# Kernel optimization log

Measured on AMD Instinct MI355X. Metric: run time of the kernel, lower is better.

## Reference

```python
import jax, jax.numpy as jnp
import numpy as np

N = 100000
D = 128      # embedding_dim
HID = 32     # hidden per head
HEADS = 4
OUT_C = 64
E = 1600000
NEG_SLOPE = 0.2


def setup_inputs() -> dict:
    key = jax.random.key(0)
    ks = jax.random.split(key, 12)
    inp = {}
    inp["x_indices"] = jnp.arange(N, dtype=jnp.int64)
    inp["ei"] = jax.random.randint(ks[0], (2, E), 0, N, dtype=jnp.int64)
    # parameters
    inp["emb"] = jax.random.normal(ks[1], (N, D), dtype=jnp.float32)
    # conv1: in=D, out=HID per head, HEADS heads, concat
    s1 = 1.0 / np.sqrt(D)
    inp["W1"] = jax.random.normal(ks[2], (D, HEADS * HID), dtype=jnp.float32) * s1
    inp["a_src1"] = jax.random.normal(ks[3], (HEADS, HID), dtype=jnp.float32) * s1
    inp["a_dst1"] = jax.random.normal(ks[4], (HEADS, HID), dtype=jnp.float32) * s1
    inp["b1"] = jnp.zeros((HEADS * HID,), dtype=jnp.float32)
    # conv2: in=HEADS*HID, out=OUT_C, 1 head
    s2 = 1.0 / np.sqrt(HEADS * HID)
    inp["W2"] = jax.random.normal(ks[5], (HEADS * HID, OUT_C), dtype=jnp.float32) * s2
    inp["a_src2"] = jax.random.normal(ks[6], (1, OUT_C), dtype=jnp.float32) * s2
    inp["a_dst2"] = jax.random.normal(ks[7], (1, OUT_C), dtype=jnp.float32) * s2
    inp["b2"] = jnp.zeros((OUT_C,), dtype=jnp.float32)
    return inp


def gat_conv(x, src, dst, W, a_src, a_dst, b, heads, out_ch, concat):
    # x: [N, Din]; src/dst: [E'] (self-loops already included)
    n = x.shape[0]
    h = (x @ W).reshape(n, heads, out_ch)          # [N, H, C]
    alpha_s = jnp.sum(h * a_src, axis=-1)          # [N, H]
    alpha_d = jnp.sum(h * a_dst, axis=-1)          # [N, H]
    e = alpha_s[src] + alpha_d[dst]                # [E', H]
    e = jnp.where(e > 0, e, NEG_SLOPE * e)         # leaky_relu
    # segment softmax over incoming edges per destination node
    m = jax.ops.segment_max(e, dst, num_segments=n)      # [N, H]
    ex = jnp.exp(e - m[dst])
    den = jax.ops.segment_sum(ex, dst, num_segments=n)   # [N, H]
    a = ex / den[dst]                              # [E', H]  (self-loops guarantee den>0)
    msg = h[src] * a[:, :, None]                   # [E', H, C]
    out = jax.ops.segment_sum(msg, dst, num_segments=n)  # [N, H, C]
    if concat:
        out = out.reshape(n, heads * out_ch)
    else:
        out = out.mean(axis=1)
    return out + b


def reference(x_indices, ei, emb, W1, a_src1, a_dst1, b1, W2, a_src2, a_dst2, b2):
    n = emb.shape[0]
    # PyG GATConv default add_self_loops=True
    loop = jnp.arange(n, dtype=ei.dtype)
    src = jnp.concatenate([ei[0], loop])
    dst = jnp.concatenate([ei[1], loop])
    x = emb[x_indices]                                  # embedding lookup
    x = jax.nn.elu(gat_conv(x, src, dst, W1, a_src1, a_dst1, b1, HEADS, HID, True))
    # dropout p=0.5 is identity in eval mode
    return gat_conv(x, src, dst, W2, a_src2, a_dst2, b2, 1, OUT_C, True)
```

## Files before the change

kernel.cpp:

```cpp
#include <hip/hip_runtime.h>
#include <math.h>

#define NEG_SLOPE 0.2f
#define BK_SHIFT 8

typedef __attribute__((ext_vector_type(2))) float v2f;

__device__ __forceinline__ float leaky(float x) { return x > 0.f ? x : NEG_SLOPE * x; }
__device__ __forceinline__ float dot4(float4 a, float4 b) {
    return a.x * b.x + a.y * b.y + a.z * b.z + a.w * b.w;
}
__device__ __forceinline__ unsigned short f2bf(float f) {
    unsigned int x = __float_as_uint(f);
    unsigned int r = (x + 0x7fffu + ((x >> 16) & 1u)) >> 16;
    return (unsigned short)r;
}
__device__ __forceinline__ float bflo(unsigned int u) { return __uint_as_float(u << 16); }
__device__ __forceinline__ float bfhi(unsigned int u) { return __uint_as_float(u & 0xffff0000u); }


__global__ void __launch_bounds__(256) bcount_kernel(const int* __restrict__ ei, int E, int E2,
                                                     int K, int* __restrict__ bcounts) {
    __shared__ int h[512];
    int t = threadIdx.x;
    h[t] = 0; h[t + 256] = 0;
    __syncthreads();
    int base = blockIdx.x * 4096;
#pragma unroll 4
    for (int i = 0; i < 16; i++) {
        int e = base + i * 256 + t;
        if (e < E2) {
            int dst = (e < E) ? ei[E + e] : (e - E);
            atomicAdd(&h[dst >> BK_SHIFT], 1);
        }
    }
    __syncthreads();
    for (int b = t; b < K; b += 256) {
        int c = h[b];
        if (c) atomicAdd(&bcounts[b], c);
    }
}

__global__ void __launch_bounds__(512) bscan_kernel(const int* __restrict__ bcounts, int K,
                                                    int* __restrict__ bbase, int* __restrict__ bcursor) {
    __shared__ int s[512];
    int t = threadIdx.x;
    int v = (t < K) ? bcounts[t] : 0;
    s[t] = v;
    __syncthreads();
    for (int off = 1; off < 512; off <<= 1) {
        int u = (t >= off) ? s[t - off] : 0;
        __syncthreads();
        s[t] += u;
        __syncthreads();
    }
    if (t < K) {
        int ex = s[t] - v;
        bbase[t] = ex;
        bcursor[t] = ex;
    }
    if (t == 511) bbase[K] = s[511];
}

__global__ void __launch_bounds__(256) bscatter_kernel(const int* __restrict__ ei, int E, int E2,
                                                       int K, int* __restrict__ bcursor,
                                                       unsigned int* __restrict__ bedges) {
    __shared__ int hist[512], pre[512], lcur[512], gbase[512], psum[256];
    __shared__ unsigned int stage[4096];
    __shared__ unsigned short binof[4096];
    int t = threadIdx.x;
    hist[t] = 0; hist[t + 256] = 0;
    __syncthreads();
    int base = blockIdx.x * 4096;
    int cnt = min(4096, E2 - base);
    int s_[16], d_[16];
#pragma unroll
    for (int i = 0; i < 16; i++) {
        int e = base + i * 256 + t;
        if (e < E2) {
            int ss, dd;
            if (e < E) { ss = ei[e]; dd = ei[E + e]; }
            else       { ss = e - E; dd = ss; }
            s_[i] = ss; d_[i] = dd;
            atomicAdd(&hist[dd >> BK_SHIFT], 1);
        }
    }
    __syncthreads();
    int a0 = hist[2 * t], a1 = hist[2 * t + 1];
    psum[t] = a0 + a1;
    __syncthreads();
    for (int off = 1; off < 256; off <<= 1) {
        int u = (t >= off) ? psum[t - off] : 0;
        __syncthreads();
        psum[t] += u;
        __syncthreads();
    }
    int pex = psum[t] - (a0 + a1);
    pre[2 * t] = pex;
    pre[2 * t + 1] = pex + a0;
    __syncthreads();
    for (int b = t; b < K; b += 256) {
        int c = hist[b];
        if (c) gbase[b] = atomicAdd(&bcursor[b], c);
    }
    lcur[t] = pre[t]; lcur[t + 256] = pre[t + 256];
    __syncthreads();
#pragma unroll
    for (int i = 0; i < 16; i++) {
        int e = base + i * 256 + t;
        if (e < E2) {
            int bin = d_[i] >> BK_SHIFT;
            int p = atomicAdd(&lcur[bin], 1);
            stage[p] = ((unsigned)s_[i] << 8) | (unsigned)(d_[i] & 255);
            binof[p] = (unsigned short)bin;
        }
    }
    __syncthreads();
    for (int i = t; i < cnt; i += 256) {
        unsigned int ed = stage[i];
        int bin = (int)binof[i];
        bedges[gbase[bin] + (i - pre[bin])] = ed;
    }
}

__global__ void __launch_bounds__(256) bcsr_kernel(const unsigned int* __restrict__ bedges,
                                                   const int* __restrict__ bbase, int N,
                                                   int* __restrict__ counts, int* __restrict__ indptr,
                                                   int* __restrict__ csr) {
    __shared__ int hist[256], scn[256], cur[256];
    int b = blockIdx.x;
    int t = threadIdx.x;
    int base = bbase[b];
    int cnt = bbase[b + 1] - base;
    hist[t] = 0;
    __syncthreads();
    for (int i = t; i < cnt; i += 256) {
        atomicAdd(&hist[bedges[base + i] & 255u], 1);
    }
    __syncthreads();
    int v = hist[t];
    scn[t] = v;
    __syncthreads();
    for (int off = 1; off < 256; off <<= 1) {
        int u = (t >= off) ? scn[t - off] : 0;
        __syncthreads();
        scn[t] += u;
        __syncthreads();
    }
    int ex = scn[t] - v;
    int d = (b << BK_SHIFT) + t;
    if (d < N) { counts[d] = v; indptr[d] = base + ex; }
    cur[t] = ex;
    __syncthreads();
    for (int i = t; i < cnt; i += 256) {
        unsigned int ed = bedges[base + i];
        int p = atomicAdd(&cur[ed & 255u], 1);
        csr[base + p] = (int)(ed >> 8);
    }
}


__global__ void w2pack_kernel(const float* __restrict__ W2, unsigned* __restrict__ w2p) {
    int i = blockIdx.x * 256 + threadIdx.x;
    if (i < 4096) {
        int k = i >> 5, j = i & 31;
        w2p[i] = (unsigned)f2bf(W2[k * 64 + 2 * j]) |
                 ((unsigned)f2bf(W2[k * 64 + 2 * j + 1]) << 16);
    }
}


__device__ __forceinline__ void fma16(float4 xv, float4 wv0, float4 wv1,
                                      float4 wv2, float4 wv3, float4& a) {
    a.x = fmaf(xv.x, wv0.x, a.x); a.y = fmaf(xv.x, wv0.y, a.y);
    a.z = fmaf(xv.x, wv0.z, a.z); a.w = fmaf(xv.x, wv0.w, a.w);
    a.x = fmaf(xv.y, wv1.x, a.x); a.y = fmaf(xv.y, wv1.y, a.y);
    a.z = fmaf(xv.y, wv1.z, a.z); a.w = fmaf(xv.y, wv1.w, a.w);
    a.x = fmaf(xv.z, wv2.x, a.x); a.y = fmaf(xv.z, wv2.y, a.y);
    a.z = fmaf(xv.z, wv2.z, a.z); a.w = fmaf(xv.z, wv2.w, a.w);
    a.x = fmaf(xv.w, wv3.x, a.x); a.y = fmaf(xv.w, wv3.y, a.y);
    a.z = fmaf(xv.w, wv3.z, a.z); a.w = fmaf(xv.w, wv3.w, a.w);
}


__global__ __launch_bounds__(256) void gemm1_kernel(const float* __restrict__ emb,
                             const int* __restrict__ xidx,
                             const float* __restrict__ W1,
                             unsigned short* __restrict__ h1b,
                             const float* __restrict__ a_s1, const float* __restrict__ a_d1,
                             float* __restrict__ as1, float* __restrict__ ad1, int N) {
    __shared__ float xs[64][64];
    __shared__ float ws[64][128];
    int tid = threadIdx.x;
    int r0 = blockIdx.x * 64;
    int tr = tid >> 5;
    int tc = tid & 31;
    float4 acc[8];
#pragma unroll
    for (int i = 0; i < 8; i++) acc[i] = make_float4(0.f, 0.f, 0.f, 0.f);
    const float4* W4 = (const float4*)W1;
    const float4* emb4 = (const float4*)emb;
    float4* ws4 = (float4*)ws;
    float4* xs4 = (float4*)xs;

    for (int half = 0; half < 2; half++) {
        float4 wbuf[8];
#pragma unroll
        for (int j = 0; j < 8; j++) wbuf[j] = W4[half * 2048 + tid + j * 256];
        float4 xbuf[4];
#pragma unroll
        for (int j = 0; j < 4; j++) {
            int idx = tid + j * 256;
            int r = idx >> 4, c = idx & 15;
            int row = r0 + r;
            float4 v = make_float4(0.f, 0.f, 0.f, 0.f);
            if (row < N) {
                int s = xidx[row];
                v = emb4[(size_t)s * 32 + half * 16 + c];
            }
            xbuf[j] = v;
        }
        __syncthreads();
#pragma unroll
        for (int j = 0; j < 8; j++) ws4[tid + j * 256] = wbuf[j];
#pragma unroll
        for (int j = 0; j < 4; j++) xs4[tid + j * 256] = xbuf[j];
        __syncthreads();
        for (int k = 0; k < 64; k += 4) {
            float4 wv0 = *(const float4*)&ws[k][tc * 4];
            float4 wv1 = *(const float4*)&ws[k + 1][tc * 4];
            float4 wv2 = *(const float4*)&ws[k + 2][tc * 4];
            float4 wv3 = *(const float4*)&ws[k + 3][tc * 4];
#pragma unroll
            for (int i = 0; i < 8; i++) {
                float4 xv = *(const float4*)&xs[tr * 8 + i][k];
                fma16(xv, wv0, wv1, wv2, wv3, acc[i]);
            }
        }
    }
    int colbase = tc * 4;
    int h = tc >> 3;
    int off = (tc & 7) * 4;
    float4 av = *(const float4*)&a_s1[h * 32 + off];
    float4 dv = *(const float4*)&a_d1[h * 32 + off];
#pragma unroll
    for (int i = 0; i < 8; i++) {
        int row = r0 + tr * 8 + i;
        if (row < N) {
            ushort4 pk;
            pk.x = f2bf(acc[i].x); pk.y = f2bf(acc[i].y);
            pk.z = f2bf(acc[i].z); pk.w = f2bf(acc[i].w);
            *(ushort4*)&h1b[(size_t)row * 128 + colbase] = pk;
        }
        float ps = dot4(acc[i], av);
        float pd = dot4(acc[i], dv);
        ps += __shfl_xor(ps, 1); pd += __shfl_xor(pd, 1);
        ps += __shfl_xor(ps, 2); pd += __shfl_xor(pd, 2);
        ps += __shfl_xor(ps, 4); pd += __shfl_xor(pd, 4);
        if ((tc & 7) == 0 && row < N) {
            as1[row * 4 + h] = ps;
            ad1[row * 4 + h] = pd;
        }
    }
}


__device__ __forceinline__ void edge_fma(uint4 u0, float w, v2f* acc) {
    v2f wv = {w, w};
    v2f t;
    t.x = bflo(u0.x); t.y = bfhi(u0.x); acc[0] += wv * t;
    t.x = bflo(u0.y); t.y = bfhi(u0.y); acc[1] += wv * t;
    t.x = bflo(u0.z); t.y = bfhi(u0.z); acc[2] += wv * t;
    t.x = bflo(u0.w); t.y = bfhi(u0.w); acc[3] += wv * t;
}

__device__ __forceinline__ void accum_tbl1(int srcReg, const float* __restrict__ ew, int mcount,
                                           const uint4* __restrict__ h1v4,
                                           int lanebase, int sub, int cg, int hh, v2f* acc) {
    int b = 0;
    for (; b + 8 <= mcount; b += 8) {
        int i0 = b + sub, i1 = b + 2 + sub, i2 = b + 4 + sub, i3 = b + 6 + sub;
        int s0 = __shfl(srcReg, lanebase + i0);
        int s1 = __shfl(srcReg, lanebase + i1);
        int s2 = __shfl(srcReg, lanebase + i2);
        int s3 = __shfl(srcReg, lanebase + i3);
        float w_0 = ew[i0 * 4 + hh];
        float w_1 = ew[i1 * 4 + hh];
        float w_2 = ew[i2 * 4 + hh];
        float w_3 = ew[i3 * 4 + hh];
        uint4 u0 = h1v4[(unsigned)(s0 * 16 + cg)];
        uint4 u1 = h1v4[(unsigned)(s1 * 16 + cg)];
        uint4 u2 = h1v4[(unsigned)(s2 * 16 + cg)];
        uint4 u3 = h1v4[(unsigned)(s3 * 16 + cg)];
        edge_fma(u0, w_0, acc);
        edge_fma(u1, w_1, acc);
        edge_fma(u2, w_2, acc);
        edge_fma(u3, w_3, acc);
    }
    if (b + 4 <= mcount) {
        int i0 = b + sub, i1 = b + 2 + sub;
        int s0 = __shfl(srcReg, lanebase + i0);
        int s1 = __shfl(srcReg, lanebase + i1);
        float w_0 = ew[i0 * 4 + hh];
        float w_1 = ew[i1 * 4 + hh];
        uint4 u0 = h1v4[(unsigned)(s0 * 16 + cg)];
        uint4 u1 = h1v4[(unsigned)(s1 * 16 + cg)];
        edge_fma(u0, w_0, acc);
        edge_fma(u1, w_1, acc);
        b += 4;
    }
    if (b + 2 <= mcount) {
        int i0 = b + sub;
        int s0 = __shfl(srcReg, lanebase + i0);
        float w_0 = ew[i0 * 4 + hh];
        uint4 u0 = h1v4[(unsigned)(s0 * 16 + cg)];
        edge_fma(u0, w_0, acc);
        b += 2;
    }
    if (b < mcount) {
        int s0 = __shfl(srcReg, lanebase + b);
        if (sub == 0) {
            float w_0 = ew[b * 4 + hh];
            uint4 u0 = h1v4[(unsigned)(s0 * 16 + cg)];
            edge_fma(u0, w_0, acc);
        }
    }
}

__global__ void __launch_bounds__(256)
agg1_kernel(const int* __restrict__ csr, const int* __restrict__ indptr,
            const int* __restrict__ counts, const float* __restrict__ as1,
            const float* __restrict__ ad1, const unsigned short* __restrict__ h1b,
            const float* __restrict__ b1, const unsigned* __restrict__ w2p,
            const float* __restrict__ a_s2, const float* __restrict__ a_d2,
            unsigned short* __restrict__ h2b, float* __restrict__ as2,
            float* __restrict__ ad2, int N) {
    __shared__ float ewt[4][2][128];
    __shared__ float xrow[4][2][128];
    __shared__ unsigned w2s[4096];
    int tid = threadIdx.x;
    {
        const uint4* w4 = (const uint4*)w2p;
        uint4* s4 = (uint4*)w2s;
        for (int i = tid; i < 1024; i += 256) s4[i] = w4[i];
    }
    __syncthreads();

    int lane = tid & 63;
    int wv = tid >> 6;
    int l32 = lane & 31;
    int lanebase = lane & 32;
    int n = blockIdx.x * 8 + wv * 2 + (lane >> 5);
    if (n < N) {
        int start = indptr[n];
        int cnt = counts[n];
        float4 ad4 = ((const float4*)ad1)[n];

        int src0 = 0;
        float4 p0 = make_float4(0.f, 0.f, 0.f, 0.f);
        if (l32 < cnt) {
            src0 = csr[start + l32];
            float4 a = ((const float4*)as1)[src0];
            p0.x = __expf(leaky(a.x + ad4.x));
            p0.y = __expf(leaky(a.y + ad4.y));
            p0.z = __expf(leaky(a.z + ad4.z));
            p0.w = __expf(leaky(a.w + ad4.w));
        }
        float4 l4 = p0;
        if (cnt > 32) {
            for (int base = 32; base < cnt; base += 32) {
                if (base + l32 < cnt) {
                    int s = csr[start + base + l32];
                    float4 a = ((const float4*)as1)[s];
                    l4.x += __expf(leaky(a.x + ad4.x));
                    l4.y += __expf(leaky(a.y + ad4.y));
                    l4.z += __expf(leaky(a.z + ad4.z));
                    l4.w += __expf(leaky(a.w + ad4.w));
                }
            }
        }
#pragma unroll
        for (int off = 16; off >= 1; off >>= 1) {
            l4.x += __shfl_xor(l4.x, off);
            l4.y += __shfl_xor(l4.y, off);
            l4.z += __shfl_xor(l4.z, off);
            l4.w += __shfl_xor(l4.w, off);
        }
        float4 li = make_float4(1.f / l4.x, 1.f / l4.y, 1.f / l4.z, 1.f / l4.w);
        float4 w0 = make_float4(p0.x * li.x, p0.y * li.y, p0.z * li.z, p0.w * li.w);

        float* ew = ewt[wv][lane >> 5];
        *(float4*)&ew[l32 * 4] = w0;

        int sub = l32 >> 4;
        int cg = lane & 15;
        int hh = cg >> 2;
        const uint4* h1v4 = (const uint4*)h1b;
        v2f acc[4];
        acc[0] = acc[1] = acc[2] = acc[3] = (v2f){0.f, 0.f};
        accum_tbl1(src0, ew, min(cnt, 32), h1v4, lanebase, sub, cg, hh, acc);
        if (cnt > 32) {
            for (int base = 32; base < cnt; base += 32) {
                int srcc = 0;
                float4 wc = make_float4(0.f, 0.f, 0.f, 0.f);
                if (base + l32 < cnt) {
                    srcc = csr[start + base + l32];
                    float4 a = ((const float4*)as1)[srcc];
                    wc.x = __expf(leaky(a.x + ad4.x)) * li.x;
                    wc.y = __expf(leaky(a.y + ad4.y)) * li.y;
                    wc.z = __expf(leaky(a.z + ad4.z)) * li.z;
                    wc.w = __expf(leaky(a.w + ad4.w)) * li.w;
                }
                *(float4*)&ew[l32 * 4] = wc;
                accum_tbl1(srcc, ew, min(cnt - base, 32), h1v4, lanebase, sub, cg, hh, acc);
            }
        }
#pragma unroll
        for (int i = 0; i < 4; i++) {
            acc[i].x += __shfl_xor(acc[i].x, 16);
            acc[i].y += __shfl_xor(acc[i].y, 16);
        }
        float* xr = xrow[wv][lane >> 5];
        if (l32 < 16) {
            const float4* b4 = (const float4*)b1;
            float4 ba = b4[cg * 2], bb = b4[cg * 2 + 1];
            float o[8];
            o[0] = acc[0].x + ba.x; o[1] = acc[0].y + ba.y;
            o[2] = acc[1].x + ba.z; o[3] = acc[1].y + ba.w;
            o[4] = acc[2].x + bb.x; o[5] = acc[2].y + bb.y;
            o[6] = acc[3].x + bb.z; o[7] = acc[3].y + bb.w;
#pragma unroll
            for (int j = 0; j < 8; j++) o[j] = (o[j] > 0.f) ? o[j] : (__expf(o[j]) - 1.f);
            *(float4*)&xr[cg * 8]     = make_float4(o[0], o[1], o[2], o[3]);
            *(float4*)&xr[cg * 8 + 4] = make_float4(o[4], o[5], o[6], o[7]);
        }
        float h0 = 0.f, h1r = 0.f;
        for (int k = 0; k < 128; k += 4) {
            float4 xv = *(const float4*)&xr[k];
            unsigned u0 = w2s[(k    ) * 32 + l32];
            unsigned u1 = w2s[(k + 1) * 32 + l32];
            unsigned u2 = w2s[(k + 2) * 32 + l32];
            unsigned u3 = w2s[(k + 3) * 32 + l32];
            h0 = fmaf(xv.x, bflo(u0), h0); h1r = fmaf(xv.x, bfhi(u0), h1r);
            h0 = fmaf(xv.y, bflo(u1), h0); h1r = fmaf(xv.y, bfhi(u1), h1r);
            h0 = fmaf(xv.z, bflo(u2), h0); h1r = fmaf(xv.z, bfhi(u2), h1r);
            h0 = fmaf(xv.w, bflo(u3), h0); h1r = fmaf(xv.w, bfhi(u3), h1r);
        }
        float2 av2 = *(const float2*)&a_s2[l32 * 2];
        float2 dv2 = *(const float2*)&a_d2[l32 * 2];
        float ps = h0 * av2.x + h1r * av2.y;
        float pd = h0 * dv2.x + h1r * dv2.y;
#pragma unroll
        for (int off = 16; off >= 1; off >>= 1) {
            ps += __shfl_xor(ps, off);
            pd += __shfl_xor(pd, off);
        }
        if (l32 == 0) { as2[n] = ps; ad2[n] = pd; }
        unsigned hp = (unsigned)f2bf(h0) | ((unsigned)f2bf(h1r) << 16);
        ((unsigned*)h2b)[(size_t)n * 32 + l32] = hp;
    }
}


__device__ __forceinline__ void accum2(int srcReg, float wReg, int mcount,
                                       const uint4* __restrict__ h2v4,
                                       int lanebase, int sub, int cg, v2f* acc) {
    int b = 0;
    for (; b + 16 <= mcount; b += 16) {
        int i0 = b + sub, i1 = b + 4 + sub, i2 = b + 8 + sub, i3 = b + 12 + sub;
        int s0 = __shfl(srcReg, lanebase + i0);
        int s1 = __shfl(srcReg, lanebase + i1);
        int s2 = __shfl(srcReg, lanebase + i2);
        int s3 = __shfl(srcReg, lanebase + i3);
        float w_0 = __shfl(wReg, lanebase + i0);
        float w_1 = __shfl(wReg, lanebase + i1);
        float w_2 = __shfl(wReg, lanebase + i2);
        float w_3 = __shfl(wReg, lanebase + i3);
        uint4 u0 = h2v4[(unsigned)(s0 * 8 + cg)];
        uint4 u1 = h2v4[(unsigned)(s1 * 8 + cg)];
        uint4 u2 = h2v4[(unsigned)(s2 * 8 + cg)];
        uint4 u3 = h2v4[(unsigned)(s3 * 8 + cg)];
        edge_fma(u0, w_0, acc);
        edge_fma(u1, w_1, acc);
        edge_fma(u2, w_2, acc);
        edge_fma(u3, w_3, acc);
    }
    if (b + 8 <= mcount) {
        int i0 = b + sub, i1 = b + 4 + sub;
        int s0 = __shfl(srcReg, lanebase + i0);
        int s1 = __shfl(srcReg, lanebase + i1);
        float w_0 = __shfl(wReg, lanebase + i0);
        float w_1 = __shfl(wReg, lanebase + i1);
        uint4 u0 = h2v4[(unsigned)(s0 * 8 + cg)];
        uint4 u1 = h2v4[(unsigned)(s1 * 8 + cg)];
        edge_fma(u0, w_0, acc);
        edge_fma(u1, w_1, acc);
        b += 8;
    }
    if (b + 4 <= mcount) {
        int i0 = b + sub;
        int s0 = __shfl(srcReg, lanebase + i0);
        float w_0 = __shfl(wReg, lanebase + i0);
        uint4 u0 = h2v4[(unsigned)(s0 * 8 + cg)];
        edge_fma(u0, w_0, acc);
        b += 4;
    }
    if (b < mcount) {
        int rem = mcount - b;
        int i0 = b + sub;
        int ic = min(i0, mcount - 1);
        int s0 = __shfl(srcReg, lanebase + ic);
        float w_0 = __shfl(wReg, lanebase + ic);
        if (sub < rem) {
            uint4 u0 = h2v4[(unsigned)(s0 * 8 + cg)];
            edge_fma(u0, w_0, acc);
        }
    }
}

__global__ void __launch_bounds__(256)
agg2_kernel(const int* __restrict__ csr, const int* __restrict__ indptr,
            const int* __restrict__ counts, const float* __restrict__ as2,
            const float* __restrict__ ad2, const unsigned short* __restrict__ h2b,
            const float* __restrict__ b2, float* __restrict__ out, int N) {
    int lane = threadIdx.x & 63;
    int l32 = lane & 31;
    int lanebase = lane & 32;
    int n = blockIdx.x * 8 + (threadIdx.x >> 6) * 2 + (lane >> 5);
    if (n >= N) return;
    int start = indptr[n];
    int cnt = counts[n];
    float ad = ad2[n];

    int src0 = 0;
    float p0 = 0.f;
    if (l32 < cnt) {
        src0 = csr[start + l32];
        p0 = __expf(leaky(as2[src0] + ad));
    }
    float l = p0;
    if (cnt > 32) {
        for (int base = 32; base < cnt; base += 32) {
            if (base + l32 < cnt)
                l += __expf(leaky(as2[csr[start + base + l32]] + ad));
        }
    }
#pragma unroll
    for (int off = 16; off >= 1; off >>= 1) l += __shfl_xor(l, off);
    float li = 1.f / l;
    float w0 = p0 * li;

    int sub = l32 >> 3;
    int cg = lane & 7;
    const uint4* h2v4 = (const uint4*)h2b;
    v2f acc[4];
    acc[0] = acc[1] = acc[2] = acc[3] = (v2f){0.f, 0.f};
    accum2(src0, w0, min(cnt, 32), h2v4, lanebase, sub, cg, acc);
    if (cnt > 32) {
        for (int base = 32; base < cnt; base += 32) {
            int srcc = 0;
            float wc = 0.f;
            if (base + l32 < cnt) {
                srcc = csr[start + base + l32];
                wc = __expf(leaky(as2[srcc] + ad)) * li;
            }
            accum2(srcc, wc, min(cnt - base, 32), h2v4, lanebase, sub, cg, acc);
        }
    }
#pragma unroll
    for (int i = 0; i < 4; i++) {
        acc[i].x += __shfl_xor(acc[i].x, 8);
        acc[i].x += __shfl_xor(acc[i].x, 16);
        acc[i].y += __shfl_xor(acc[i].y, 8);
        acc[i].y += __shfl_xor(acc[i].y, 16);
    }
    if (l32 < 8) {
        const float4* b4 = (const float4*)b2;
        float4 ba = b4[cg * 2], bb = b4[cg * 2 + 1];
        float4 o0, o1;
        o0.x = acc[0].x + ba.x; o0.y = acc[0].y + ba.y;
        o0.z = acc[1].x + ba.z; o0.w = acc[1].y + ba.w;
        o1.x = acc[2].x + bb.x; o1.y = acc[2].y + bb.y;
        o1.z = acc[3].x + bb.z; o1.w = acc[3].y + bb.w;
        float4* orow = (float4*)&out[(size_t)n * 64 + cg * 8];
        orow[0] = o0;
        orow[1] = o1;
    }
}


extern "C" void kernel_launch(void* const* d_in, const int* in_sizes, int n_in,
                              void* d_out, int out_size, void* d_ws, size_t ws_size,
                              hipStream_t stream) {
    const int*   xidx = (const int*)d_in[0];
    const int*   ei   = (const int*)d_in[1];
    const float* emb  = (const float*)d_in[2];
    const float* W1   = (const float*)d_in[3];
    const float* a_s1 = (const float*)d_in[4];
    const float* a_d1 = (const float*)d_in[5];
    const float* b1   = (const float*)d_in[6];
    const float* W2   = (const float*)d_in[7];
    const float* a_s2 = (const float*)d_in[8];
    const float* a_d2 = (const float*)d_in[9];
    const float* b2   = (const float*)d_in[10];
    float* out = (float*)d_out;

    const int N  = in_sizes[0];
    const int E  = in_sizes[1] / 2;
    const int E2 = E + N;
    const int K  = (N + 255) >> BK_SHIFT;

    int* ws_i    = (int*)d_ws;
    int* counts  = ws_i;
    int* indptr  = ws_i + N;
    int* bcounts = ws_i + 2 * (size_t)N;
    int* bbase   = ws_i + 2 * (size_t)N + 512;
    int* bcursor = ws_i + 2 * (size_t)N + 1032;
    int* csr     = ws_i + 2 * (size_t)N + 1544;
    size_t fbase = ((size_t)(2 * (size_t)N + 1544 + E2) + 3) & ~(size_t)3;
    float* ws_f = (float*)d_ws;
    unsigned short* h1b = (unsigned short*)(ws_f + fbase);
    float* region2 = ws_f + fbase + (size_t)N * 64;
    unsigned short* h2b = (unsigned short*)region2;
    float* as2 = region2 + (size_t)N * 32;
    float* ad2 = region2 + (size_t)N * 33;
    unsigned* w2p = (unsigned*)(region2 + (size_t)N * 34);
    float* as1 = ws_f + fbase + (size_t)N * 128;
    float* ad1 = as1 + (size_t)N * 4;
    unsigned int* bedges = (unsigned int*)region2;

    int nchunks = (E2 + 4095) / 4096;
    hipMemsetAsync(bcounts, 0, (size_t)K * sizeof(int), stream);
    bcount_kernel<<<nchunks, 256, 0, stream>>>(ei, E, E2, K, bcounts);
    bscan_kernel<<<1, 512, 0, stream>>>(bcounts, K, bbase, bcursor);
    bscatter_kernel<<<nchunks, 256, 0, stream>>>(ei, E, E2, K, bcursor, bedges);
    bcsr_kernel<<<K, 256, 0, stream>>>(bedges, bbase, N, counts, indptr, csr);

    gemm1_kernel<<<(N + 63) / 64, 256, 0, stream>>>(emb, xidx, W1, h1b, a_s1, a_d1, as1, ad1, N);

    w2pack_kernel<<<16, 256, 0, stream>>>(W2, w2p);

    agg1_kernel<<<(N + 7) / 8, 256, 0, stream>>>(csr, indptr, counts, as1, ad1, h1b, b1,
                                                 w2p, a_s2, a_d2, h2b, as2, ad2, N);

    agg2_kernel<<<(N + 7) / 8, 256, 0, stream>>>(csr, indptr, counts, as2, ad2, h2b, b2, out, N);
}
```

Baseline: 405.6 us.

## Compute fused layer-2 projection in agg1 with bf16 MFMA instead of scalar FMAs

Replaces the per-lane scalar FMA loop for the fused x·W2 projection in agg1 with 16x16x32 bf16 MFMA instructions. Each wave packs its two node rows as bf16 into shared memory, reusing the edge-weight buffer, and pre-swizzles W2 into the MFMA B-operand layout. Bounds checks are restructured so whole waves stay convergent for the MFMA. The matrix unit runs only 2 of 16 rows, so most of its work is padding. The ELU output is now rounded to bf16 before the projection, which adds precision loss.

```diff
diff --git a/kernel.cpp b/kernel.cpp
--- a/kernel.cpp
+++ b/kernel.cpp
@@ -5,6 +5,8 @@
 #define BK_SHIFT 8
 
 typedef __attribute__((ext_vector_type(2))) float v2f;
+typedef __attribute__((ext_vector_type(8))) short bf16x8;
+typedef __attribute__((ext_vector_type(4))) float f32x4;
 
 __device__ __forceinline__ float leaky(float x) { return x > 0.f ? x : NEG_SLOPE * x; }
 __device__ __forceinline__ float dot4(float4 a, float4 b) {
@@ -160,12 +162,16 @@
 }
 
 
-__global__ void w2pack_kernel(const float* __restrict__ W2, unsigned* __restrict__ w2p) {
+__global__ void w2pack_kernel(const float* __restrict__ W2, unsigned short* __restrict__ w2p) {
     int i = blockIdx.x * 256 + threadIdx.x;
-    if (i < 4096) {
-        int k = i >> 5, j = i & 31;
-        w2p[i] = (unsigned)f2bf(W2[k * 64 + 2 * j]) |
-                 ((unsigned)f2bf(W2[k * 64 + 2 * j + 1]) << 16);
+    if (i < 8192) {
+        int t = i >> 11;
+        int c = (i >> 9) & 3;
+        int l = (i >> 3) & 63;
+        int j = i & 7;
+        int k = t * 32 + (l >> 4) * 8 + j;
+        int col = c * 16 + (l & 15);
+        w2p[i] = f2bf(W2[k * 64 + col]);
     }
 }
 
@@ -331,13 +337,12 @@
 agg1_kernel(const int* __restrict__ csr, const int* __restrict__ indptr,
             const int* __restrict__ counts, const float* __restrict__ as1,
             const float* __restrict__ ad1, const unsigned short* __restrict__ h1b,
-            const float* __restrict__ b1, const unsigned* __restrict__ w2p,
+            const float* __restrict__ b1, const unsigned short* __restrict__ w2p,
             const float* __restrict__ a_s2, const float* __restrict__ a_d2,
             unsigned short* __restrict__ h2b, float* __restrict__ as2,
             float* __restrict__ ad2, int N) {
-    __shared__ float ewt[4][2][128];
-    __shared__ float xrow[4][2][128];
-    __shared__ unsigned w2s[4096];
+    __shared__ __attribute__((aligned(16))) float ewt[4][2][128];
+    __shared__ __attribute__((aligned(16))) unsigned short w2s[8192];
     int tid = threadIdx.x;
     {
         const uint4* w4 = (const uint4*)w2p;
@@ -351,113 +356,134 @@
     int l32 = lane & 31;
     int lanebase = lane & 32;
     int n = blockIdx.x * 8 + wv * 2 + (lane >> 5);
-    if (n < N) {
-        int start = indptr[n];
-        int cnt = counts[n];
-        float4 ad4 = ((const float4*)ad1)[n];
-
-        int src0 = 0;
-        float4 p0 = make_float4(0.f, 0.f, 0.f, 0.f);
-        if (l32 < cnt) {
-            src0 = csr[start + l32];
-            float4 a = ((const float4*)as1)[src0];
-            p0.x = __expf(leaky(a.x + ad4.x));
-            p0.y = __expf(leaky(a.y + ad4.y));
-            p0.z = __expf(leaky(a.z + ad4.z));
-            p0.w = __expf(leaky(a.w + ad4.w));
-        }
-        float4 l4 = p0;
-        if (cnt > 32) {
-            for (int base = 32; base < cnt; base += 32) {
-                if (base + l32 < cnt) {
-                    int s = csr[start + base + l32];
-                    float4 a = ((const float4*)as1)[s];
-                    l4.x += __expf(leaky(a.x + ad4.x));
-                    l4.y += __expf(leaky(a.y + ad4.y));
-                    l4.z += __expf(leaky(a.z + ad4.z));
-                    l4.w += __expf(leaky(a.w + ad4.w));
-                }
+    bool valid = (n < N);
+    int nsafe = valid ? n : 0;
+    int start = indptr[nsafe];
+    int cnt = valid ? counts[nsafe] : 0;
+    float4 ad4 = ((const float4*)ad1)[nsafe];
+
+    int src0 = 0;
+    float4 p0 = make_float4(0.f, 0.f, 0.f, 0.f);
+    if (l32 < cnt) {
+        src0 = csr[start + l32];
+        float4 a = ((const float4*)as1)[src0];
+        p0.x = __expf(leaky(a.x + ad4.x));
+        p0.y = __expf(leaky(a.y + ad4.y));
+        p0.z = __expf(leaky(a.z + ad4.z));
+        p0.w = __expf(leaky(a.w + ad4.w));
+    }
+    float4 l4 = p0;
+    if (cnt > 32) {
+        for (int base = 32; base < cnt; base += 32) {
+            if (base + l32 < cnt) {
+                int s = csr[start + base + l32];
+                float4 a = ((const float4*)as1)[s];
+                l4.x += __expf(leaky(a.x + ad4.x));
+                l4.y += __expf(leaky(a.y + ad4.y));
+                l4.z += __expf(leaky(a.z + ad4.z));
+                l4.w += __expf(leaky(a.w + ad4.w));
             }
         }
-#pragma unroll
-        for (int off = 16; off >= 1; off >>= 1) {
-            l4.x += __shfl_xor(l4.x, off);
-            l4.y += __shfl_xor(l4.y, off);
-            l4.z += __shfl_xor(l4.z, off);
-            l4.w += __shfl_xor(l4.w, off);
-        }
-        float4 li = make_float4(1.f / l4.x, 1.f / l4.y, 1.f / l4.z, 1.f / l4.w);
-        float4 w0 = make_float4(p0.x * li.x, p0.y * li.y, p0.z * li.z, p0.w * li.w);
-
-        float* ew = ewt[wv][lane >> 5];
-        *(float4*)&ew[l32 * 4] = w0;
-
-        int sub = l32 >> 4;
-        int cg = lane & 15;
-        int hh = cg >> 2;
-        const uint4* h1v4 = (const uint4*)h1b;
-        v2f acc[4];
-        acc[0] = acc[1] = acc[2] = acc[3] = (v2f){0.f, 0.f};
-        accum_tbl1(src0, ew, min(cnt, 32), h1v4, lanebase, sub, cg, hh, acc);
-        if (cnt > 32) {
-            for (int base = 32; base < cnt; base += 32) {
-                int srcc = 0;
-                float4 wc = make_float4(0.f, 0.f, 0.f, 0.f);
-                if (base + l32 < cnt) {
-                    srcc = csr[start + base + l32];
-                    float4 a = ((const float4*)as1)[srcc];
-                    wc.x = __expf(leaky(a.x + ad4.x)) * li.x;
-                    wc.y = __expf(leaky(a.y + ad4.y)) * li.y;
-                    wc.z = __expf(leaky(a.z + ad4.z)) * li.z;
-                    wc.w = __expf(leaky(a.w + ad4.w)) * li.w;
-                }
-                *(float4*)&ew[l32 * 4] = wc;
-                accum_tbl1(srcc, ew, min(cnt - base, 32), h1v4, lanebase, sub, cg, hh, acc);
+    }
+#pragma unroll
+    for (int off = 16; off >= 1; off >>= 1) {
+        l4.x += __shfl_xor(l4.x, off);
+        l4.y += __shfl_xor(l4.y, off);
+        l4.z += __shfl_xor(l4.z, off);
+        l4.w += __shfl_xor(l4.w, off);
+    }
+    float4 li = make_float4(1.f / l4.x, 1.f / l4.y, 1.f / l4.z, 1.f / l4.w);
+    float4 w0 = make_float4(p0.x * li.x, p0.y * li.y, p0.z * li.z, p0.w * li.w);
+
+    float* ew = ewt[wv][lane >> 5];
+    *(float4*)&ew[l32 * 4] = w0;
+
+    int sub = l32 >> 4;
+    int cg = lane & 15;
+    int hh = cg >> 2;
+    const uint4* h1v4 = (const uint4*)h1b;
+    v2f acc[4];
+    acc[0] = acc[1] = acc[2] = acc[3] = (v2f){0.f, 0.f};
+    accum_tbl1(src0, ew, min(cnt, 32), h1v4, lanebase, sub, cg, hh, acc);
+    if (cnt > 32) {
+        for (int base = 32; base < cnt; base += 32) {
+            int srcc = 0;
+            float4 wc = make_float4(0.f, 0.f, 0.f, 0.f);
+            if (base + l32 < cnt) {
+                srcc = csr[start + base + l32];
+                float4 a = ((const float4*)as1)[srcc];
+                wc.x = __expf(leaky(a.x + ad4.x)) * li.x;
+                wc.y = __expf(leaky(a.y + ad4.y)) * li.y;
+                wc.z = __expf(leaky(a.z + ad4.z)) * li.z;
+                wc.w = __expf(leaky(a.w + ad4.w)) * li.w;
             }
-        }
-#pragma unroll
-        for (int i = 0; i < 4; i++) {
-            acc[i].x += __shfl_xor(acc[i].x, 16);
-            acc[i].y += __shfl_xor(acc[i].y, 16);
-        }
-        float* xr = xrow[wv][lane >> 5];
-        if (l32 < 16) {
-            const float4* b4 = (const float4*)b1;
-            float4 ba = b4[cg * 2], bb = b4[cg * 2 + 1];
-            float o[8];
-            o[0] = acc[0].x + ba.x; o[1] = acc[0].y + ba.y;
-            o[2] = acc[1].x + ba.z; o[3] = acc[1].y + ba.w;
-            o[4] = acc[2].x + bb.x; o[5] = acc[2].y + bb.y;
-            o[6] = acc[3].x + bb.z; o[7] = acc[3].y + bb.w;
-#pragma unroll
-            for (int j = 0; j < 8; j++) o[j] = (o[j] > 0.f) ? o[j] : (__expf(o[j]) - 1.f);
-            *(float4*)&xr[cg * 8]     = make_float4(o[0], o[1], o[2], o[3]);
-            *(float4*)&xr[cg * 8 + 4] = make_float4(o[4], o[5], o[6], o[7]);
-        }
-        float h0 = 0.f, h1r = 0.f;
-        for (int k = 0; k < 128; k += 4) {
-            float4 xv = *(const float4*)&xr[k];
-            unsigned u0 = w2s[(k    ) * 32 + l32];
-            unsigned u1 = w2s[(k + 1) * 32 + l32];
-            unsigned u2 = w2s[(k + 2) * 32 + l32];
-            unsigned u3 = w2s[(k + 3) * 32 + l32];
-            h0 = fmaf(xv.x, bflo(u0), h0); h1r = fmaf(xv.x, bfhi(u0), h1r);
-            h0 = fmaf(xv.y, bflo(u1), h0); h1r = fmaf(xv.y, bfhi(u1), h1r);
-            h0 = fmaf(xv.z, bflo(u2), h0); h1r = fmaf(xv.z, bfhi(u2), h1r);
-            h0 = fmaf(xv.w, bflo(u3), h0); h1r = fmaf(xv.w, bfhi(u3), h1r);
-        }
-        float2 av2 = *(const float2*)&a_s2[l32 * 2];
-        float2 dv2 = *(const float2*)&a_d2[l32 * 2];
-        float ps = h0 * av2.x + h1r * av2.y;
-        float pd = h0 * dv2.x + h1r * dv2.y;
-#pragma unroll
-        for (int off = 16; off >= 1; off >>= 1) {
-            ps += __shfl_xor(ps, off);
-            pd += __shfl_xor(pd, off);
-        }
-        if (l32 == 0) { as2[n] = ps; ad2[n] = pd; }
-        unsigned hp = (unsigned)f2bf(h0) | ((unsigned)f2bf(h1r) << 16);
-        ((unsigned*)h2b)[(size_t)n * 32 + l32] = hp;
+            *(float4*)&ew[l32 * 4] = wc;
+            accum_tbl1(srcc, ew, min(cnt - base, 32), h1v4, lanebase, sub, cg, hh, acc);
+        }
+    }
+#pragma unroll
+    for (int i = 0; i < 4; i++) {
+        acc[i].x += __shfl_xor(acc[i].x, 16);
+        acc[i].y += __shfl_xor(acc[i].y, 16);
+    }
+    unsigned short* xa = (unsigned short*)&ewt[wv][0][0];
+    if (l32 < 16) {
+        const float4* b4 = (const float4*)b1;
+        float4 ba = b4[cg * 2], bb = b4[cg * 2 + 1];
+        float o[8];
+        o[0] = acc[0].x + ba.x; o[1] = acc[0].y + ba.y;
+        o[2] = acc[1].x + ba.z; o[3] = acc[1].y + ba.w;
+        o[4] = acc[2].x + bb.x; o[5] = acc[2].y + bb.y;
+        o[6] = acc[3].x + bb.z; o[7] = acc[3].y + bb.w;
+#pragma unroll
+        for (int j = 0; j < 8; j++) o[j] = (o[j] > 0.f) ? o[j] : (__expf(o[j]) - 1.f);
+        uint4 pk;
+        pk.x = (unsigned)f2bf(o[0]) | ((unsigned)f2bf(o[1]) << 16);
+        pk.y = (unsigned)f2bf(o[2]) | ((unsigned)f2bf(o[3]) << 16);
+        pk.z = (unsigned)f2bf(o[4]) | ((unsigned)f2bf(o[5]) << 16);
+        pk.w = (unsigned)f2bf(o[6]) | ((unsigned)f2bf(o[7]) << 16);
+        *(uint4*)&xa[cg * 16 + (lane >> 5) * 8] = pk;
+    }
+    int rowA = lane & 15;
+    int kb = lane >> 4;
+    f32x4 hacc[4];
+#pragma unroll
+    for (int c = 0; c < 4; c++) hacc[c] = (f32x4){0.f, 0.f, 0.f, 0.f};
+#pragma unroll
+    for (int t = 0; t < 4; t++) {
+        bf16x8 af = {0, 0, 0, 0, 0, 0, 0, 0};
+        if (rowA < 2) af = *(const bf16x8*)&xa[(t * 4 + kb) * 16 + rowA * 8];
+#pragma unroll
+        for (int c = 0; c < 4; c++) {
+            bf16x8 bf = *(const bf16x8*)&w2s[((t * 4 + c) * 64 + lane) * 8];
+            hacc[c] = __builtin_amdgcn_mfma_f32_16x16x32_bf16(af, bf, hacc[c], 0, 0, 0);
+        }
+    }
+    int na = blockIdx.x * 8 + wv * 2;
+    int nb = na + 1;
+    bool va = (na < N), vb = (nb < N);
+    if (lane < 16) {
+        float psa = 0.f, pda = 0.f, psb = 0.f, pdb = 0.f;
+#pragma unroll
+        for (int c = 0; c < 4; c++) {
+            float h0 = hacc[c][0];
+            float h1r = hacc[c][1];
+            float asv = a_s2[c * 16 + lane];
+            float adv = a_d2[c * 16 + lane];
+            psa = fmaf(h0, asv, psa); pda = fmaf(h0, adv, pda);
+            psb = fmaf(h1r, asv, psb); pdb = fmaf(h1r, adv, pdb);
+            if (va) h2b[(size_t)na * 64 + c * 16 + lane] = f2bf(h0);
+            if (vb) h2b[(size_t)nb * 64 + c * 16 + lane] = f2bf(h1r);
+        }
+#pragma unroll
+        for (int off = 8; off >= 1; off >>= 1) {
+            psa += __shfl_xor(psa, off); pda += __shfl_xor(pda, off);
+            psb += __shfl_xor(psb, off); pdb += __shfl_xor(pdb, off);
+        }
+        if (lane == 0) {
+            if (va) { as2[na] = psa; ad2[na] = pda; }
+            if (vb) { as2[nb] = psb; ad2[nb] = pdb; }
+        }
     }
 }
 
@@ -624,7 +650,7 @@
     unsigned short* h2b = (unsigned short*)region2;
     float* as2 = region2 + (size_t)N * 32;
     float* ad2 = region2 + (size_t)N * 33;
-    unsigned* w2p = (unsigned*)(region2 + (size_t)N * 34);
+    unsigned short* w2p = (unsigned short*)(region2 + (size_t)N * 34);
     float* as1 = ws_f + fbase + (size_t)N * 128;
     float* ad1 = as1 + (size_t)N * 4;
     unsigned int* bedges = (unsigned int*)region2;
@@ -638,7 +664,7 @@
 
     gemm1_kernel<<<(N + 63) / 64, 256, 0, stream>>>(emb, xidx, W1, h1b, a_s1, a_d1, as1, ad1, N);
 
-    w2pack_kernel<<<16, 256, 0, stream>>>(W2, w2p);
+    w2pack_kernel<<<32, 256, 0, stream>>>(W2, w2p);
 
     agg1_kernel<<<(N + 7) / 8, 256, 0, stream>>>(csr, indptr, counts, as1, ad1, h1b, b1,
                                                  w2p, a_s2, a_d2, h2b, as2, ad2, N);
```

Measured after the change: 401.3 us. No clear change (-1.1%).
